# Optimization experiments

Hardware: AMD Instinct MI355X
Metric: run time of the kernel (lower is better)

Reference implementation:

```python
import jax, jax.numpy as jnp
import numpy as np

NUM_USERS = 8000
NUM_ITEMS = 4000
EMB_DIM = 64
NUM_LAYERS = 3
NUM_EDGES = 300000
N = NUM_USERS + NUM_ITEMS


def setup_inputs() -> dict:
    key = jax.random.key(0)
    k1, k2, k3 = jax.random.split(key, 3)
    edge_index = jax.random.randint(k1, (2, NUM_EDGES), 0, N, dtype=jnp.int64 if jax.config.jax_enable_x64 else jnp.int32)
    # xavier-uniform-like init
    bound = float(np.sqrt(6.0 / (NUM_USERS + EMB_DIM)))
    user_emb = jax.random.uniform(k2, (NUM_USERS, EMB_DIM), jnp.float32, -bound, bound)
    bound_i = float(np.sqrt(6.0 / (NUM_ITEMS + EMB_DIM)))
    item_emb = jax.random.uniform(k3, (NUM_ITEMS, EMB_DIM), jnp.float32, -bound_i, bound_i)
    return {"edge_index": edge_index, "user_emb": user_emb, "item_emb": item_emb}


def _normalized_adj(edge_index):
    # dense symmetric adjacency from edge list, then D^{-1/2} A D^{-1/2}
    adj = jnp.zeros((N, N), jnp.float32)
    adj = adj.at[edge_index[0], edge_index[1]].set(1.0)
    adj = adj.at[edge_index[1], edge_index[0]].set(1.0)
    degree = jnp.clip(adj.sum(axis=1, keepdims=True), 1.0)  # (N,1)
    dsqrt = jnp.sqrt(degree)
    return adj / dsqrt / dsqrt.T


def reference(edge_index, user_emb, item_emb):
    adj = _normalized_adj(edge_index)
    all_emb = jnp.concatenate([user_emb, item_emb], axis=0)  # (N, d)
    acc = all_emb
    cur = all_emb
    for _ in range(NUM_LAYERS):
        cur = adj @ cur
        acc = acc + cur
    final = acc / (NUM_LAYERS + 1)  # mean over layer outputs
    return final[:NUM_USERS], final[NUM_USERS:]
```

## Files before the change

kernel.cpp:

```cpp
#include <hip/hip_runtime.h>
#include <hip/hip_bf16.h>

namespace {

constexpr int NU = 8000;
constexpr int NI = 4000;
constexpr int NN = 12000;
constexpr int D  = 64;
constexpr int NE = 300000;
constexpr int STRIDE = 128;

__device__ __forceinline__ int probe_e32(const unsigned* raw, int lane) {
    unsigned v = raw[2 * lane + 1];
    return (__ballot(v != 0u) != 0ull) ? 1 : 0;
}
__device__ __forceinline__ int probe_f32(const unsigned short* ue, int lane) {
    int e = (ue[2 * lane] >> 7) & 0xFF;
    return (__ballot(e > 126) != 0ull) ? 1 : 0;
}

__global__ __launch_bounds__(256) void scatter_init(const unsigned* __restrict__ raw,
                                                    const unsigned short* __restrict__ ue,
                                                    const unsigned short* __restrict__ ie,
                                                    int* __restrict__ fill,
                                                    int* __restrict__ col,
                                                    unsigned short* __restrict__ x0,
                                                    float* __restrict__ out) {
    const int tid  = blockIdx.x * blockDim.x + threadIdx.x;
    const int NT   = gridDim.x * blockDim.x;
    const int lane = threadIdx.x & 63;
    const int e32  = probe_e32(raw, lane);
    const int f32  = probe_f32(ue, lane);

    for (int t = tid; t < NE; t += NT) {
        int a, b;
        if (e32) { a = (int)raw[t];     b = (int)raw[NE + t]; }
        else     { a = (int)raw[2 * t]; b = (int)raw[2 * NE + 2 * t]; }
        int s = atomicAdd(&fill[a], 1);
        if (s < STRIDE) col[a * STRIDE + s] = b;
        if (a != b) {
            s = atomicAdd(&fill[b], 1);
            if (s < STRIDE) col[b * STRIDE + s] = a;
        }
    }
    for (int q = tid; q < NN * D / 4; q += NT) {
        int i = q * 4;
        float4 vf;
        ushort4 vb;
        if (f32) {
            const float* src = (i < NU * D) ? ((const float*)ue) + i
                                            : ((const float*)ie) + (i - NU * D);
            vf = *(const float4*)src;
            vb.x = (unsigned short)(__bfloat16_as_ushort(__float2bfloat16(vf.x)));
            vb.y = (unsigned short)(__bfloat16_as_ushort(__float2bfloat16(vf.y)));
            vb.z = (unsigned short)(__bfloat16_as_ushort(__float2bfloat16(vf.z)));
            vb.w = (unsigned short)(__bfloat16_as_ushort(__float2bfloat16(vf.w)));
        } else {
            const unsigned short* src = (i < NU * D) ? ue + i : ie + (i - NU * D);
            vb = *(const ushort4*)src;
            vf.x = __uint_as_float(((unsigned)vb.x) << 16);
            vf.y = __uint_as_float(((unsigned)vb.y) << 16);
            vf.z = __uint_as_float(((unsigned)vb.z) << 16);
            vf.w = __uint_as_float(((unsigned)vb.w) << 16);
        }
        *(ushort4*)(x0 + i) = vb;
        *(float4*)(out + i) = vf;
    }
}

__global__ __launch_bounds__(64) void dedup(const int* __restrict__ fill,
                                            int* __restrict__ col,
                                            int* __restrict__ degu,
                                            float* __restrict__ dinv) {
    __shared__ unsigned bits[376];
    __shared__ int cnt;
    const int row = blockIdx.x, lane = threadIdx.x;
    for (int w = lane; w < 376; w += 64) bits[w] = 0;
    if (lane == 0) cnt = 0;
    __syncthreads();
    int n = fill[row]; n = n < STRIDE ? n : STRIDE;
    const int base = row * STRIDE;
    for (int cb = 0; cb < n; cb += 64) {
        int idx = cb + lane;
        if (idx < n) {
            int c = col[base + idx];
            unsigned bit = 1u << (c & 31);
            unsigned old = atomicOr(&bits[c >> 5], bit);
            if (!(old & bit)) {
                int pos = atomicAdd(&cnt, 1);
                col[base + pos] = c;
            }
        }
    }
    __syncthreads();
    if (lane == 0) {
        int d = cnt;
        degu[row] = d;
        dinv[row] = rsqrtf((float)(d > 0 ? d : 1));
    }
}

__global__ __launch_bounds__(64) void spmm(const int* __restrict__ degu,
                                           const float* __restrict__ dinv,
                                           const int* __restrict__ col,
                                           const unsigned short* __restrict__ xin,
                                           unsigned short* __restrict__ xout,
                                           float* __restrict__ out,
                                           int final_layer) {
    const int row  = blockIdx.x;
    const int lane = threadIdx.x;
    const int n    = degu[row];
    const int base = row * STRIDE;
    const float dr = dinv[row];
    float sum = 0.f;
    #pragma unroll 4
    for (int j = 0; j < n; ++j) {
        int   c = col[base + j];
        float w = dr * dinv[c];
        float v = __uint_as_float(((unsigned)xin[c * D + lane]) << 16);
        sum = fmaf(w, v, sum);
    }
    const int o = row * D + lane;
    if (final_layer) {
        out[o] = (out[o] + sum) * 0.25f;
    } else {
        xout[o] = (unsigned short)__bfloat16_as_ushort(__float2bfloat16(sum));
        out[o] += sum;
    }
}

}

extern "C" void kernel_launch(void* const* d_in, const int* in_sizes, int n_in,
                              void* d_out, int out_size, void* d_ws, size_t ws_size,
                              hipStream_t stream) {
    int ei = 0, ui = 1, ii = 2;
    for (int i = 0; i < n_in; ++i) {
        if      (in_sizes[i] == 2 * NE) ei = i;
        else if (in_sizes[i] == NU * D) ui = i;
        else if (in_sizes[i] == NI * D) ii = i;
    }
    const unsigned*       raw = (const unsigned*)d_in[ei];
    const unsigned short* ue  = (const unsigned short*)d_in[ui];
    const unsigned short* ie  = (const unsigned short*)d_in[ii];
    float*                out = (float*)d_out;

    char* ws = (char*)d_ws;
    size_t off = 0;
    auto take = [&](size_t bytes) {
        void* p = ws + off;
        off += (bytes + 15) & ~(size_t)15;
        return p;
    };
    int*            fill = (int*)take(NN * 4);
    int*            degu = (int*)take(NN * 4);
    float*          dinv = (float*)take(NN * 4);
    int*            col  = (int*)take((size_t)NN * STRIDE * 4);
    unsigned short* x0   = (unsigned short*)take((size_t)NN * D * 2);
    unsigned short* x1   = (unsigned short*)take((size_t)NN * D * 2);
    (void)ws_size;

    hipMemsetAsync(fill, 0, NN * 4, stream);
    scatter_init<<<1024, 256, 0, stream>>>(raw, ue, ie, fill, col, x0, out);
    dedup<<<NN, 64, 0, stream>>>(fill, col, degu, dinv);

    spmm<<<NN, 64, 0, stream>>>(degu, dinv, col, x0, x1, out, 0);
    spmm<<<NN, 64, 0, stream>>>(degu, dinv, col, x1, x0, out, 0);
    spmm<<<NN, 64, 0, stream>>>(degu, dinv, col, x0, nullptr, out, 1);
}
```

Before: 151.3 us.

## Fuse CSR build and dedup into one block-local shared-memory kernel

Replaces the global-atomic edge scatter, separate dedup kernel and memset with a single kernel where each block owns a range of rows, scans all edges, and bins neighbors into shared memory before deduplicating per wave with ballot-based compaction. This removes global atomics, the memset, and one launch. In exchange every block rereads the entire edge list, and only 120 blocks run, risking low occupancy and redundant traffic.

Measured after the change: 530.8 us. +250.8%, slower.

```diff
diff --git a/kernel.cpp b/kernel.cpp
--- a/kernel.cpp
+++ b/kernel.cpp
@@ -9,6 +9,8 @@
 constexpr int D  = 64;
 constexpr int NE = 300000;
 constexpr int STRIDE = 128;
+constexpr int RPB = 100;
+constexpr int BBLOCKS = NN / RPB;
 
 __device__ __forceinline__ int probe_e32(const unsigned* raw, int lane) {
     unsigned v = raw[2 * lane + 1];
@@ -19,31 +21,74 @@
     return (__ballot(e > 126) != 0ull) ? 1 : 0;
 }
 
-__global__ __launch_bounds__(256) void scatter_init(const unsigned* __restrict__ raw,
-                                                    const unsigned short* __restrict__ ue,
-                                                    const unsigned short* __restrict__ ie,
-                                                    int* __restrict__ fill,
-                                                    int* __restrict__ col,
-                                                    unsigned short* __restrict__ x0,
-                                                    float* __restrict__ out) {
-    const int tid  = blockIdx.x * blockDim.x + threadIdx.x;
-    const int NT   = gridDim.x * blockDim.x;
-    const int lane = threadIdx.x & 63;
+__global__ __launch_bounds__(256) void build(const unsigned* __restrict__ raw,
+                                             const unsigned short* __restrict__ ue,
+                                             const unsigned short* __restrict__ ie,
+                                             int* __restrict__ col,
+                                             int* __restrict__ degu,
+                                             float* __restrict__ dinv,
+                                             unsigned short* __restrict__ x0,
+                                             float* __restrict__ out) {
+    __shared__ unsigned short lcol[RPB][STRIDE];
+    __shared__ int lcnt[RPB];
+    __shared__ unsigned bits[4][376];
+    const int tid  = threadIdx.x;
+    const int wave = tid >> 6, lane = tid & 63;
+    const int row0 = blockIdx.x * RPB;
     const int e32  = probe_e32(raw, lane);
     const int f32  = probe_f32(ue, lane);
 
-    for (int t = tid; t < NE; t += NT) {
+    for (int i = tid; i < RPB; i += 256) lcnt[i] = 0;
+    __syncthreads();
+
+    for (int t = tid; t < NE; t += 256) {
         int a, b;
         if (e32) { a = (int)raw[t];     b = (int)raw[NE + t]; }
         else     { a = (int)raw[2 * t]; b = (int)raw[2 * NE + 2 * t]; }
-        int s = atomicAdd(&fill[a], 1);
-        if (s < STRIDE) col[a * STRIDE + s] = b;
-        if (a != b) {
-            s = atomicAdd(&fill[b], 1);
-            if (s < STRIDE) col[b * STRIDE + s] = a;
+        int ra = a - row0;
+        if ((unsigned)ra < (unsigned)RPB) {
+            int s = atomicAdd(&lcnt[ra], 1);
+            if (s < STRIDE) lcol[ra][s] = (unsigned short)b;
+        }
+        int rb = b - row0;
+        if (b != a && (unsigned)rb < (unsigned)RPB) {
+            int s = atomicAdd(&lcnt[rb], 1);
+            if (s < STRIDE) lcol[rb][s] = (unsigned short)a;
         }
     }
-    for (int q = tid; q < NN * D / 4; q += NT) {
+    __syncthreads();
+
+    for (int r = wave; r < RPB; r += 4) {
+        unsigned* bb = bits[wave];
+        for (int w = lane; w < 376; w += 64) bb[w] = 0;
+        int n = lcnt[r]; n = n < STRIDE ? n : STRIDE;
+        int uniq = 0;
+        const int grow = row0 + r;
+        for (int cb = 0; cb < n; cb += 64) {
+            int idx = cb + lane;
+            int pos = -1, c = 0;
+            if (idx < n) {
+                c = (int)lcol[r][idx];
+                unsigned bit = 1u << (c & 31);
+                unsigned old = atomicOr(&bb[c >> 5], bit);
+                if (!(old & bit)) pos = 1;
+            }
+            unsigned long long m = __ballot(pos > 0);
+            if (pos > 0) {
+                int myoff = __popcll(m & ((1ull << lane) - 1ull));
+                col[grow * STRIDE + uniq + myoff] = c;
+            }
+            uniq += __popcll(m);
+        }
+        if (lane == 0) {
+            degu[grow] = uniq;
+            dinv[grow] = rsqrtf((float)(uniq > 0 ? uniq : 1));
+        }
+    }
+
+    const int gtid = blockIdx.x * 256 + tid;
+    const int NT   = BBLOCKS * 256;
+    for (int q = gtid; q < NN * D / 4; q += NT) {
         int i = q * 4;
         float4 vf;
         ushort4 vb;
@@ -51,10 +96,10 @@
             const float* src = (i < NU * D) ? ((const float*)ue) + i
                                             : ((const float*)ie) + (i - NU * D);
             vf = *(const float4*)src;
-            vb.x = (unsigned short)(__bfloat16_as_ushort(__float2bfloat16(vf.x)));
-            vb.y = (unsigned short)(__bfloat16_as_ushort(__float2bfloat16(vf.y)));
-            vb.z = (unsigned short)(__bfloat16_as_ushort(__float2bfloat16(vf.z)));
-            vb.w = (unsigned short)(__bfloat16_as_ushort(__float2bfloat16(vf.w)));
+            vb.x = __bfloat16_as_ushort(__float2bfloat16(vf.x));
+            vb.y = __bfloat16_as_ushort(__float2bfloat16(vf.y));
+            vb.z = __bfloat16_as_ushort(__float2bfloat16(vf.z));
+            vb.w = __bfloat16_as_ushort(__float2bfloat16(vf.w));
         } else {
             const unsigned short* src = (i < NU * D) ? ue + i : ie + (i - NU * D);
             vb = *(const ushort4*)src;
@@ -65,38 +110,6 @@
         }
         *(ushort4*)(x0 + i) = vb;
         *(float4*)(out + i) = vf;
-    }
-}
-
-__global__ __launch_bounds__(64) void dedup(const int* __restrict__ fill,
-                                            int* __restrict__ col,
-                                            int* __restrict__ degu,
-                                            float* __restrict__ dinv) {
-    __shared__ unsigned bits[376];
-    __shared__ int cnt;
-    const int row = blockIdx.x, lane = threadIdx.x;
-    for (int w = lane; w < 376; w += 64) bits[w] = 0;
-    if (lane == 0) cnt = 0;
-    __syncthreads();
-    int n = fill[row]; n = n < STRIDE ? n : STRIDE;
-    const int base = row * STRIDE;
-    for (int cb = 0; cb < n; cb += 64) {
-        int idx = cb + lane;
-        if (idx < n) {
-            int c = col[base + idx];
-            unsigned bit = 1u << (c & 31);
-            unsigned old = atomicOr(&bits[c >> 5], bit);
-            if (!(old & bit)) {
-                int pos = atomicAdd(&cnt, 1);
-                col[base + pos] = c;
-            }
-        }
-    }
-    __syncthreads();
-    if (lane == 0) {
-        int d = cnt;
-        degu[row] = d;
-        dinv[row] = rsqrtf((float)(d > 0 ? d : 1));
     }
 }
 
@@ -152,7 +165,6 @@
         off += (bytes + 15) & ~(size_t)15;
         return p;
     };
-    int*            fill = (int*)take(NN * 4);
     int*            degu = (int*)take(NN * 4);
     float*          dinv = (float*)take(NN * 4);
     int*            col  = (int*)take((size_t)NN * STRIDE * 4);
@@ -160,9 +172,7 @@
     unsigned short* x1   = (unsigned short*)take((size_t)NN * D * 2);
     (void)ws_size;
 
-    hipMemsetAsync(fill, 0, NN * 4, stream);
-    scatter_init<<<1024, 256, 0, stream>>>(raw, ue, ie, fill, col, x0, out);
-    dedup<<<NN, 64, 0, stream>>>(fill, col, degu, dinv);
+    build<<<BBLOCKS, 256, 0, stream>>>(raw, ue, ie, col, degu, dinv, x0, out);
 
     spmm<<<NN, 64, 0, stream>>>(degu, dinv, col, x0, x1, out, 0);
     spmm<<<NN, 64, 0, stream>>>(degu, dinv, col, x1, x0, out, 0);
```

## Pack four rows per block and process two neighbors per wave in SpMM

Applied to the files above, without the earlier changes.

Dedup and SpMM now map one wavefront per row with four rows per 256-thread block, which cuts the block count by a factor of four. Dedup replaces the shared atomic counter and block barrier with a ballot/popcount compaction inside the wave. In SpMM each half-wave handles a different neighbor and loads packed bf16 pairs, so every iteration covers two edges; the two halves are then combined with a shuffle and written back as float2. This halves the serial loop length per row, at the cost of a few extra selects and a cross-lane reduction.

New measurement: 185.5 us. 22.6% more time.

```diff
diff --git a/kernel.cpp b/kernel.cpp
--- a/kernel.cpp
+++ b/kernel.cpp
@@ -51,10 +51,10 @@
             const float* src = (i < NU * D) ? ((const float*)ue) + i
                                             : ((const float*)ie) + (i - NU * D);
             vf = *(const float4*)src;
-            vb.x = (unsigned short)(__bfloat16_as_ushort(__float2bfloat16(vf.x)));
-            vb.y = (unsigned short)(__bfloat16_as_ushort(__float2bfloat16(vf.y)));
-            vb.z = (unsigned short)(__bfloat16_as_ushort(__float2bfloat16(vf.z)));
-            vb.w = (unsigned short)(__bfloat16_as_ushort(__float2bfloat16(vf.w)));
+            vb.x = __bfloat16_as_ushort(__float2bfloat16(vf.x));
+            vb.y = __bfloat16_as_ushort(__float2bfloat16(vf.y));
+            vb.z = __bfloat16_as_ushort(__float2bfloat16(vf.z));
+            vb.w = __bfloat16_as_ushort(__float2bfloat16(vf.w));
         } else {
             const unsigned short* src = (i < NU * D) ? ue + i : ie + (i - NU * D);
             vb = *(const ushort4*)src;
@@ -68,64 +68,91 @@
     }
 }
 
-__global__ __launch_bounds__(64) void dedup(const int* __restrict__ fill,
-                                            int* __restrict__ col,
-                                            int* __restrict__ degu,
-                                            float* __restrict__ dinv) {
-    __shared__ unsigned bits[376];
-    __shared__ int cnt;
-    const int row = blockIdx.x, lane = threadIdx.x;
-    for (int w = lane; w < 376; w += 64) bits[w] = 0;
-    if (lane == 0) cnt = 0;
-    __syncthreads();
+__global__ __launch_bounds__(256) void dedup(const int* __restrict__ fill,
+                                             int* __restrict__ col,
+                                             int* __restrict__ degu,
+                                             float* __restrict__ dinv) {
+    __shared__ unsigned bits[4][376];
+    const int lane = threadIdx.x & 63;
+    const int wave = __builtin_amdgcn_readfirstlane(threadIdx.x >> 6);
+    const int row  = blockIdx.x * 4 + wave;
+    unsigned* bb = bits[wave];
+    for (int w = lane; w < 376; w += 64) bb[w] = 0;
     int n = fill[row]; n = n < STRIDE ? n : STRIDE;
     const int base = row * STRIDE;
+    int uniq = 0;
     for (int cb = 0; cb < n; cb += 64) {
         int idx = cb + lane;
+        int c = 0;
+        bool win = false;
         if (idx < n) {
-            int c = col[base + idx];
+            c = col[base + idx];
             unsigned bit = 1u << (c & 31);
-            unsigned old = atomicOr(&bits[c >> 5], bit);
-            if (!(old & bit)) {
-                int pos = atomicAdd(&cnt, 1);
-                col[base + pos] = c;
-            }
+            unsigned old = atomicOr(&bb[c >> 5], bit);
+            win = !(old & bit);
         }
+        unsigned long long m = __ballot(win);
+        if (win) {
+            int myoff = __popcll(m & ((1ull << lane) - 1ull));
+            col[base + uniq + myoff] = c;
+        }
+        uniq += __popcll(m);
     }
-    __syncthreads();
     if (lane == 0) {
-        int d = cnt;
-        degu[row] = d;
-        dinv[row] = rsqrtf((float)(d > 0 ? d : 1));
+        degu[row] = uniq;
+        dinv[row] = rsqrtf((float)(uniq > 0 ? uniq : 1));
     }
 }
 
-__global__ __launch_bounds__(64) void spmm(const int* __restrict__ degu,
-                                           const float* __restrict__ dinv,
-                                           const int* __restrict__ col,
-                                           const unsigned short* __restrict__ xin,
-                                           unsigned short* __restrict__ xout,
-                                           float* __restrict__ out,
-                                           int final_layer) {
-    const int row  = blockIdx.x;
-    const int lane = threadIdx.x;
+__global__ __launch_bounds__(256) void spmm(const int* __restrict__ degu,
+                                            const float* __restrict__ dinv,
+                                            const int* __restrict__ col,
+                                            const unsigned short* __restrict__ xin,
+                                            unsigned short* __restrict__ xout,
+                                            float* __restrict__ out,
+                                            int final_layer) {
+    const int lane = threadIdx.x & 63;
+    const int wave = __builtin_amdgcn_readfirstlane(threadIdx.x >> 6);
+    const int row  = blockIdx.x * 4 + wave;
+    const int half = lane >> 5;
+    const int sub  = lane & 31;
     const int n    = degu[row];
     const int base = row * STRIDE;
     const float dr = dinv[row];
-    float sum = 0.f;
-    #pragma unroll 4
-    for (int j = 0; j < n; ++j) {
-        int   c = col[base + j];
-        float w = dr * dinv[c];
-        float v = __uint_as_float(((unsigned)xin[c * D + lane]) << 16);
-        sum = fmaf(w, v, sum);
+    float sum0 = 0.f, sum1 = 0.f;
+    for (int j = 0; j < n; j += 2) {
+        int j1 = j + 1 < n ? j + 1 : j;
+        int c0 = col[base + j];
+        int c1 = col[base + j1];
+        float w0 = dr * dinv[c0];
+        float w1 = (j + 1 < n) ? dr * dinv[c1] : 0.f;
+        int   c = half ? c1 : c0;
+        float w = half ? w1 : w0;
+        unsigned u = *(const unsigned*)(xin + c * D + 2 * sub);
+        float lo = __uint_as_float(u << 16);
+        float hi = __uint_as_float(u & 0xFFFF0000u);
+        sum0 = fmaf(w, lo, sum0);
+        sum1 = fmaf(w, hi, sum1);
     }
-    const int o = row * D + lane;
-    if (final_layer) {
-        out[o] = (out[o] + sum) * 0.25f;
-    } else {
-        xout[o] = (unsigned short)__bfloat16_as_ushort(__float2bfloat16(sum));
-        out[o] += sum;
+    sum0 += __shfl(sum0, lane ^ 32, 64);
+    sum1 += __shfl(sum1, lane ^ 32, 64);
+    if (lane < 32) {
+        const int o2 = row * D + 2 * sub;
+        float2 prev = *(const float2*)(out + o2);
+        if (final_layer) {
+            float2 r;
+            r.x = (prev.x + sum0) * 0.25f;
+            r.y = (prev.y + sum1) * 0.25f;
+            *(float2*)(out + o2) = r;
+        } else {
+            unsigned plo = (unsigned)__bfloat16_as_ushort(__float2bfloat16(sum0));
+            unsigned phi = (unsigned)__bfloat16_as_ushort(__float2bfloat16(sum1));
+            *(unsigned*)(xout + o2) = plo | (phi << 16);
+            float2 r;
+            r.x = prev.x + sum0;
+            r.y = prev.y + sum1;
+            *(float2*)(out + o2) = r;
+        }
     }
 }
 
@@ -162,9 +189,9 @@
 
     hipMemsetAsync(fill, 0, NN * 4, stream);
     scatter_init<<<1024, 256, 0, stream>>>(raw, ue, ie, fill, col, x0, out);
-    dedup<<<NN, 64, 0, stream>>>(fill, col, degu, dinv);
+    dedup<<<NN / 4, 256, 0, stream>>>(fill, col, degu, dinv);
 
-    spmm<<<NN, 64, 0, stream>>>(degu, dinv, col, x0, x1, out, 0);
-    spmm<<<NN, 64, 0, stream>>>(degu, dinv, col, x1, x0, out, 0);
-    spmm<<<NN, 64, 0, stream>>>(degu, dinv, col, x0, nullptr, out, 1);
+    spmm<<<NN / 4, 256, 0, stream>>>(degu, dinv, col, x0, x1, out, 0);
+    spmm<<<NN / 4, 256, 0, stream>>>(degu, dinv, col, x1, x0, out, 0);
+    spmm<<<NN / 4, 256, 0, stream>>>(degu, dinv, col, x0, nullptr, out, 1);
 }
```
